# Performance work log

Measured on AMD Instinct MI355X. Metric: run time of the kernel, lower is better.

## Reference

```python
import jax, jax.numpy as jnp
import numpy as np
import math

E_IN, E_OUT = 512, 96
B, QL, PL = 64, 128, 196

def _lin(k, shape):
    fan_in = shape[1]
    bound = 1.0 / math.sqrt(fan_in)
    k1, k2 = jax.random.split(k)
    W = jax.random.uniform(k1, shape, jnp.float32, -bound, bound)
    b = jax.random.uniform(k2, (shape[0],), jnp.float32, -bound, bound)
    return W, b

def setup_inputs() -> dict:
    key = jax.random.key(0)
    ks = jax.random.split(key, 16)
    inp = {
        'z_d_cls': jax.random.normal(ks[0], (B, E_IN), jnp.float32),
        'Z_d_tok': jax.random.normal(ks[1], (B, QL, E_IN), jnp.float32),
        'z_t_cls': jax.random.normal(ks[2], (B, E_IN), jnp.float32),
        'Z_t_tok': jax.random.normal(ks[3], (B, QL, E_IN), jnp.float32),
        'z_v_cls': jax.random.normal(ks[4], (B, E_IN), jnp.float32),
        'Z_v_patch': jax.random.normal(ks[5], (B, PL, E_IN), jnp.float32),
    }
    names = ['t_cls', 'd_cls', 'v_cls', 't_tok', 'v_patch', 'tgl_q', 'tgl_k', 'tgl_v']
    for i, n in enumerate(names):
        W, b = _lin(ks[6 + i], (E_OUT, E_IN))
        inp[f'W_{n}'] = W
        inp[f'b_{n}'] = b
    inp['ln_g'] = jnp.ones((E_OUT,), jnp.float32)
    inp['ln_b'] = jnp.zeros((E_OUT,), jnp.float32)
    return inp

def _l2n(x, eps=1e-6):
    return x / jnp.maximum(jnp.linalg.norm(x, axis=-1, keepdims=True), eps)

def _proj(x, W, b):
    return x @ W.T + b

def _layer_norm(x, g, b, eps=1e-5):
    mu = jnp.mean(x, axis=-1, keepdims=True)
    var = jnp.mean((x - mu) ** 2, axis=-1, keepdims=True)
    return (x - mu) / jnp.sqrt(var + eps) * g + b

def reference(z_d_cls, Z_d_tok, z_t_cls, Z_t_tok, z_v_cls, Z_v_patch,
              W_t_cls, b_t_cls, W_d_cls, b_d_cls, W_v_cls, b_v_cls,
              W_t_tok, b_t_tok, W_v_patch, b_v_patch,
              W_tgl_q, b_tgl_q, W_tgl_k, b_tgl_k, W_tgl_v, b_tgl_v,
              ln_g, ln_b):
    # --- TGG: global-global text/doc cosine sim [B, B]
    t = _l2n(_proj(z_t_cls, W_t_cls, b_t_cls))
    d = _l2n(_proj(z_d_cls, W_d_cls, b_d_cls))
    S_TGG = t @ d.T
    # --- TGL: cross-attention over all batch pairs
    Q = _proj(Z_d_tok, W_tgl_q, b_tgl_q)   # [b, q, h]
    K = _proj(Z_t_tok, W_tgl_k, b_tgl_k)   # [c, k, h]
    V = _proj(Z_t_tok, W_tgl_v, b_tgl_v)   # [c, k, h]
    scores = jnp.einsum('bqh,ckh->bcqk', Q, K) / math.sqrt(E_OUT)
    attn = jax.nn.softmax(scores, axis=-1)
    context = jnp.einsum('bcqk,ckh->bcqh', attn, V).mean(axis=2)  # [b, c, h]
    context = _layer_norm(context, ln_g, ln_b)
    S_TGL = jnp.einsum('ih,ijh->ij', d, _l2n(context))
    S_TIB = 0.5 * (S_TGG + S_TGL)
    # --- CGG: global-global text/vision cosine sim
    v = _l2n(_proj(z_v_cls, W_v_cls, b_v_cls))
    S_CGG = t @ v.T
    # --- CLL: token-patch max similarity
    t_tok = _l2n(_proj(Z_t_tok, W_t_tok, b_t_tok))        # [b, t, h]
    v_pat = _l2n(_proj(Z_v_patch, W_v_patch, b_v_patch))  # [c, p, h]
    sim = jnp.einsum('bth,cph->bctp', t_tok, v_pat)
    S_CLL = sim.max(axis=(-1, -2))
    S_CAB = 0.5 * (S_CGG + S_CLL)
    return S_TIB + S_CAB
```

## Files before the change

### kernel.cpp

```cpp
#include <hip/hip_runtime.h>
#include <hip/hip_bf16.h>

typedef __bf16 bf16;
typedef __attribute__((ext_vector_type(8))) __bf16 bf16x8;
typedef __attribute__((ext_vector_type(4))) float f32x4;
typedef __attribute__((ext_vector_type(4))) unsigned int uint4v;

#define MFMA16(a, b, c) __builtin_amdgcn_mfma_f32_16x16x32_bf16(a, b, c, 0, 0, 0)

__device__ inline bf16x8 cvt8(const float* p) {
    f32x4 lo = *(const f32x4*)p;
    f32x4 hi = *(const f32x4*)(p + 4);
    bf16x8 r;
    r[0] = (bf16)lo[0]; r[1] = (bf16)lo[1]; r[2] = (bf16)lo[2]; r[3] = (bf16)lo[3];
    r[4] = (bf16)hi[0]; r[5] = (bf16)hi[1]; r[6] = (bf16)hi[2]; r[7] = (bf16)hi[3];
    return r;
}


struct WPtrs { const float* W[8]; };

__global__ __launch_bounds__(256) void cvtw_kernel(WPtrs wp, bf16* __restrict__ Wb) {
    int j   = blockIdx.x / 48;
    int blk = blockIdx.x - j * 48;
    int idx = (blk * 256 + threadIdx.x) * 4;
    f32x4 v = *(const f32x4*)(wp.W[j] + idx);
    bf16* dst = Wb + j * 49152 + idx;
    dst[0] = (bf16)v[0]; dst[1] = (bf16)v[1]; dst[2] = (bf16)v[2]; dst[3] = (bf16)v[3];
}


struct ProjParams {
    const float* src[8];
    const float* B[8];
    void* dst[8];
    const bf16* Wb;
};

__global__ __launch_bounds__(256, 3) void proj_kernel(ProjParams p) {
    int wid  = (blockIdx.x << 2) + (threadIdx.x >> 6);
    if (wid >= 1422) return;
    int lane = threadIdx.x & 63;
    int m = lane & 15, quad = lane >> 4;

    int job = 0, base = 0;
    if (wid >= 2)    { job = 1; base = 2; }
    if (wid >= 4)    { job = 2; base = 4; }
    if (wid >= 6)    { job = 3; base = 6; }
    if (wid >= 262)  { job = 4; base = 262; }
    if (wid >= 518)  { job = 5; base = 518; }
    if (wid >= 774)  { job = 6; base = 774; }
    if (wid >= 1030) { job = 7; base = 1030; }
    int wtile = wid - base;
    int r0 = wtile << 5;

    const float* X  = p.src[job];
    const bf16*  wb = p.Wb + job * 49152 + (size_t)m * 512 + quad * 8;
    const float* x0 = X + (size_t)(r0 + m) * 512 + quad * 8;
    const float* x1 = x0 + 16 * 512;

    f32x4 acc[2][6] = {};
    #pragma unroll 4
    for (int kk = 0; kk < 512; kk += 32) {
        bf16x8 a0 = cvt8(x0 + kk);
        bf16x8 a1 = cvt8(x1 + kk);
        #pragma unroll
        for (int nt = 0; nt < 6; nt++) {
            bf16x8 b = *(const bf16x8*)(wb + nt * 8192 + kk);
            acc[0][nt] = MFMA16(a0, b, acc[0][nt]);
            acc[1][nt] = MFMA16(a1, b, acc[1][nt]);
        }
    }
    const float* Bv = p.B[job];
    bool norm = (job < 3) || (job >= 6);
    #pragma unroll
    for (int t2 = 0; t2 < 2; t2++) {
        int row0 = r0 + t2 * 16;
        f32x4* a = acc[t2];
        #pragma unroll
        for (int nt = 0; nt < 6; nt++) {
            float bb = Bv[nt * 16 + m];
            a[nt][0] += bb; a[nt][1] += bb; a[nt][2] += bb; a[nt][3] += bb;
        }
        if (norm) {
            #pragma unroll
            for (int r = 0; r < 4; r++) {
                float ss = 0.0f;
                #pragma unroll
                for (int nt = 0; nt < 6; nt++) ss += a[nt][r] * a[nt][r];
                ss += __shfl_xor(ss, 1); ss += __shfl_xor(ss, 2);
                ss += __shfl_xor(ss, 4); ss += __shfl_xor(ss, 8);
                float inv = 1.0f / fmaxf(sqrtf(ss), 1e-6f);
                #pragma unroll
                for (int nt = 0; nt < 6; nt++) a[nt][r] *= inv;
            }
        }
        if (job < 3) {
            float* dst = (float*)p.dst[job];
            #pragma unroll
            for (int r = 0; r < 4; r++)
                #pragma unroll
                for (int nt = 0; nt < 6; nt++)
                    dst[(size_t)(row0 + quad * 4 + r) * 96 + nt * 16 + m] = a[nt][r];
        } else {
            bf16* dst = (bf16*)p.dst[job];
            #pragma unroll
            for (int r = 0; r < 4; r++)
                #pragma unroll
                for (int nt = 0; nt < 6; nt++)
                    dst[(size_t)(row0 + quad * 4 + r) * 96 + nt * 16 + m] = (bf16)a[nt][r];
        }
    }
}


__global__ __launch_bounds__(256, 3) void attn_kernel(
    const bf16* __restrict__ Qg, const bf16* __restrict__ Kg, const bf16* __restrict__ Vg,
    const float* __restrict__ dvec, const float* __restrict__ ln_g, const float* __restrict__ ln_b,
    float* __restrict__ S_TGL)
{
    int b = blockIdx.x >> 6, c = blockIdx.x & 63;
    int tid = threadIdx.x, lane = tid & 63, w = tid >> 6;
    int m = lane & 15, quad = lane >> 4;
    const bf16* Q = Qg + (size_t)b * (128 * 96);
    const bf16* K = Kg + (size_t)c * (128 * 96);
    const bf16* V = Vg + (size_t)c * (128 * 96);

    __shared__ __align__(16) bf16 Klds[128 * 96];
    #pragma unroll
    for (int ch = 0; ch < 6; ch++) {
        int idx = (ch * 256 + tid) * 8;
        *(uint4v*)(Klds + idx) = *(const uint4v*)(K + idx);
    }
    __syncthreads();

    f32x4 acc[2][8] = {};
    #pragma unroll
    for (int kk = 0; kk < 96; kk += 32) {
        bf16x8 a0 = *(const bf16x8*)(Q + (size_t)(w * 32 + m) * 96 + kk + quad * 8);
        bf16x8 a1 = *(const bf16x8*)(Q + (size_t)(w * 32 + 16 + m) * 96 + kk + quad * 8);
        #pragma unroll
        for (int nt = 0; nt < 8; nt++) {
            bf16x8 bb = *(const bf16x8*)(Klds + (nt * 16 + m) * 96 + kk + quad * 8);
            acc[0][nt] = MFMA16(a0, bb, acc[0][nt]);
            acc[1][nt] = MFMA16(a1, bb, acc[1][nt]);
        }
    }
    const float sc = 0.10206207261596575f;
    float wpart[8];
    #pragma unroll
    for (int nt = 0; nt < 8; nt++) wpart[nt] = 0.0f;
    #pragma unroll
    for (int mt = 0; mt < 2; mt++) {
        #pragma unroll
        for (int r = 0; r < 4; r++) {
            float tv[8]; float mx = -3.4e38f;
            #pragma unroll
            for (int nt = 0; nt < 8; nt++) { tv[nt] = acc[mt][nt][r] * sc; mx = fmaxf(mx, tv[nt]); }
            mx = fmaxf(mx, __shfl_xor(mx, 1)); mx = fmaxf(mx, __shfl_xor(mx, 2));
            mx = fmaxf(mx, __shfl_xor(mx, 4)); mx = fmaxf(mx, __shfl_xor(mx, 8));
            float s = 0.0f;
            #pragma unroll
            for (int nt = 0; nt < 8; nt++) { tv[nt] = __expf(tv[nt] - mx); s += tv[nt]; }
            s += __shfl_xor(s, 1); s += __shfl_xor(s, 2);
            s += __shfl_xor(s, 4); s += __shfl_xor(s, 8);
            float inv = 1.0f / s;
            #pragma unroll
            for (int nt = 0; nt < 8; nt++) wpart[nt] += tv[nt] * inv;
        }
    }
    #pragma unroll
    for (int nt = 0; nt < 8; nt++) {
        wpart[nt] += __shfl_xor(wpart[nt], 16);
        wpart[nt] += __shfl_xor(wpart[nt], 32);
    }
    __shared__ float wsum4[4][128];
    __shared__ float wk[128];
    __shared__ float ctx[96];
    if (lane < 16) {
        #pragma unroll
        for (int nt = 0; nt < 8; nt++) wsum4[w][nt * 16 + lane] = wpart[nt];
    }
    __syncthreads();
    if (tid < 128) wk[tid] = wsum4[0][tid] + wsum4[1][tid] + wsum4[2][tid] + wsum4[3][tid];
    __syncthreads();
    if (tid < 96) {
        float a = 0.0f;
        for (int k = 0; k < 128; k++) a += wk[k] * (float)V[(size_t)k * 96 + tid];
        ctx[tid] = a * (1.0f / 128.0f);
    }
    __syncthreads();
    if (w == 0) {
        float x0 = ctx[lane];
        float x1 = (lane < 32) ? ctx[64 + lane] : 0.0f;
        float s = x0 + x1;
        #pragma unroll
        for (int d = 1; d < 64; d <<= 1) s += __shfl_xor(s, d);
        float mean = s * (1.0f / 96.0f);
        float e0 = x0 - mean;
        float e1 = (lane < 32) ? (x1 - mean) : 0.0f;
        float q = e0 * e0 + e1 * e1;
        #pragma unroll
        for (int d = 1; d < 64; d <<= 1) q += __shfl_xor(q, d);
        float rstd = rsqrtf(q * (1.0f / 96.0f) + 1e-5f);
        float y0 = e0 * rstd * ln_g[lane] + ln_b[lane];
        float y1 = 0.0f;
        if (lane < 32) y1 = e1 * rstd * ln_g[64 + lane] + ln_b[64 + lane];
        const float* db = dvec + b * 96;
        float dot = y0 * db[lane] + ((lane < 32) ? y1 * db[64 + lane] : 0.0f);
        float ss = y0 * y0 + y1 * y1;
        #pragma unroll
        for (int d = 1; d < 64; d <<= 1) { dot += __shfl_xor(dot, d); ss += __shfl_xor(ss, d); }
        if (lane == 0) S_TGL[blockIdx.x] = dot / fmaxf(sqrtf(ss), 1e-6f);
    }
}


__global__ __launch_bounds__(256, 3) void cll_kernel(
    const bf16* __restrict__ Tt, const bf16* __restrict__ Vp, float* __restrict__ S_CLL)
{
    int b = blockIdx.x >> 6, c = blockIdx.x & 63;
    int tid = threadIdx.x, lane = tid & 63, w = tid >> 6;
    int m = lane & 15, quad = lane >> 4;
    const bf16* T = Tt + (size_t)b * (128 * 96);
    const bf16* P = Vp + (size_t)c * (196 * 96);

    __shared__ __align__(16) bf16 Plds[196 * 96];
    for (int ch = tid; ch < 2352; ch += 256)
        *(uint4v*)(Plds + ch * 8) = *(const uint4v*)(P + ch * 8);
    __syncthreads();

    int rofs[13];
    #pragma unroll
    for (int nt = 0; nt < 13; nt++) {
        int r = nt * 16 + m; if (r > 195) r = 195;
        rofs[nt] = r * 96;
    }
    f32x4 acc[2][13] = {};
    #pragma unroll
    for (int kk = 0; kk < 96; kk += 32) {
        bf16x8 a0 = *(const bf16x8*)(T + (size_t)(w * 32 + m) * 96 + kk + quad * 8);
        bf16x8 a1 = *(const bf16x8*)(T + (size_t)(w * 32 + 16 + m) * 96 + kk + quad * 8);
        #pragma unroll
        for (int nt = 0; nt < 13; nt++) {
            bf16x8 bb = *(const bf16x8*)(Plds + rofs[nt] + kk + quad * 8);
            acc[0][nt] = MFMA16(a0, bb, acc[0][nt]);
            acc[1][nt] = MFMA16(a1, bb, acc[1][nt]);
        }
    }
    float mx = -3.4e38f;
    #pragma unroll
    for (int mt = 0; mt < 2; mt++)
        #pragma unroll
        for (int nt = 0; nt < 13; nt++)
            #pragma unroll
            for (int r = 0; r < 4; r++) mx = fmaxf(mx, acc[mt][nt][r]);
    #pragma unroll
    for (int d = 1; d < 64; d <<= 1) mx = fmaxf(mx, __shfl_xor(mx, d));
    __shared__ float red[4];
    if (lane == 0) red[w] = mx;
    __syncthreads();
    if (tid == 0) S_CLL[blockIdx.x] = fmaxf(fmaxf(red[0], red[1]), fmaxf(red[2], red[3]));
}


__global__ __launch_bounds__(64) void final_kernel(
    const float* __restrict__ t, const float* __restrict__ d, const float* __restrict__ v,
    const float* __restrict__ S_TGL, const float* __restrict__ S_CLL, float* __restrict__ out)
{
    int i = blockIdx.x, j = threadIdx.x;
    __shared__ float ti[96];
    if (j < 64) ti[j] = t[i * 96 + j];
    if (j < 32) ti[64 + j] = t[i * 96 + 64 + j];
    __syncthreads();
    float tg = 0.0f, cg = 0.0f;
    const float* dj = d + j * 96;
    const float* vj = v + j * 96;
    #pragma unroll 8
    for (int h = 0; h < 96; h++) { float th = ti[h]; tg += th * dj[h]; cg += th * vj[h]; }
    float res = 0.5f * (tg + S_TGL[i * 64 + j]) + 0.5f * (cg + S_CLL[i * 64 + j]);
    out[i * 64 + j] = res;
}


extern "C" void kernel_launch(void* const* d_in, const int* in_sizes, int n_in,
                              void* d_out, int out_size, void* d_ws, size_t ws_size,
                              hipStream_t stream)
{
    (void)in_sizes; (void)n_in; (void)out_size; (void)ws_size;
    const float* z_d_cls   = (const float*)d_in[0];
    const float* Z_d_tok   = (const float*)d_in[1];
    const float* z_t_cls   = (const float*)d_in[2];
    const float* Z_t_tok   = (const float*)d_in[3];
    const float* z_v_cls   = (const float*)d_in[4];
    const float* Z_v_patch = (const float*)d_in[5];

    char* ws = (char*)d_ws;
    float* t     = (float*)(ws + 0);
    float* d     = (float*)(ws + 24576);
    float* v     = (float*)(ws + 49152);
    float* S_TGL = (float*)(ws + 73728);
    float* S_CLL = (float*)(ws + 90112);
    bf16* Wb = (bf16*)(ws + 106496);
    bf16* Qb = (bf16*)(ws + 892928);
    bf16* Kb = (bf16*)(ws + 892928 + 1572864);
    bf16* Vb = (bf16*)(ws + 892928 + 2 * 1572864);
    bf16* Tt = (bf16*)(ws + 892928 + 3 * 1572864);
    bf16* Vp = (bf16*)(ws + 892928 + 4 * 1572864);

    WPtrs wp;
    wp.W[0] = (const float*)d_in[6];
    wp.W[1] = (const float*)d_in[8];
    wp.W[2] = (const float*)d_in[10];
    wp.W[3] = (const float*)d_in[16];
    wp.W[4] = (const float*)d_in[18];
    wp.W[5] = (const float*)d_in[20];
    wp.W[6] = (const float*)d_in[12];
    wp.W[7] = (const float*)d_in[14];
    hipLaunchKernelGGL(cvtw_kernel, dim3(384), dim3(256), 0, stream, wp, Wb);

    ProjParams pp;
    pp.Wb = Wb;
    pp.src[0] = z_t_cls;   pp.B[0] = (const float*)d_in[7];  pp.dst[0] = t;
    pp.src[1] = z_d_cls;   pp.B[1] = (const float*)d_in[9];  pp.dst[1] = d;
    pp.src[2] = z_v_cls;   pp.B[2] = (const float*)d_in[11]; pp.dst[2] = v;
    pp.src[3] = Z_d_tok;   pp.B[3] = (const float*)d_in[17]; pp.dst[3] = Qb;
    pp.src[4] = Z_t_tok;   pp.B[4] = (const float*)d_in[19]; pp.dst[4] = Kb;
    pp.src[5] = Z_t_tok;   pp.B[5] = (const float*)d_in[21]; pp.dst[5] = Vb;
    pp.src[6] = Z_t_tok;   pp.B[6] = (const float*)d_in[13]; pp.dst[6] = Tt;
    pp.src[7] = Z_v_patch; pp.B[7] = (const float*)d_in[15]; pp.dst[7] = Vp;
    hipLaunchKernelGGL(proj_kernel, dim3(356), dim3(256), 0, stream, pp);

    hipLaunchKernelGGL(attn_kernel, dim3(4096), dim3(256), 0, stream,
                       (const bf16*)Qb, (const bf16*)Kb, (const bf16*)Vb,
                       (const float*)d, (const float*)d_in[22], (const float*)d_in[23], S_TGL);
    hipLaunchKernelGGL(cll_kernel, dim3(4096), dim3(256), 0, stream,
                       (const bf16*)Tt, (const bf16*)Vp, S_CLL);
    hipLaunchKernelGGL(final_kernel, dim3(64), dim3(64), 0, stream,
                       (const float*)t, (const float*)d, (const float*)v,
                       (const float*)S_TGL, (const float*)S_CLL, (float*)d_out);
}
```

Measured before the change: 254.1 us.

## Split projection N across two waves, pad LDS rows, parallelize attention V reduction

The projection kernel now uses 128-thread blocks in which two waves each compute half of the 96 output columns for a 32-row tile. The row L2 norm is combined across the two waves through shared memory, and the grid grows to 1422 blocks for more parallelism. The attention and CLL kernels pad their LDS rows from 96 to 104 bf16 elements to avoid bank conflicts on MFMA operand loads, and both drop the min-blocks occupancy hint. The attention context reduction over V now runs on all four waves with paired bf16 loads instead of a serial 128-step loop on 96 threads, at the cost of an extra sync and a small partial-sum buffer.

```diff
diff --git a/kernel.cpp b/kernel.cpp
--- a/kernel.cpp
+++ b/kernel.cpp
@@ -37,84 +37,105 @@
     const bf16* Wb;
 };
 
-__global__ __launch_bounds__(256, 3) void proj_kernel(ProjParams p) {
-    int wid  = (blockIdx.x << 2) + (threadIdx.x >> 6);
-    if (wid >= 1422) return;
-    int lane = threadIdx.x & 63;
+__global__ __launch_bounds__(128, 8) void proj_kernel(ProjParams p) {
+    int g   = blockIdx.x;
+    int tid = threadIdx.x;
+    int nh = tid >> 6, lane = tid & 63;
     int m = lane & 15, quad = lane >> 4;
 
     int job = 0, base = 0;
-    if (wid >= 2)    { job = 1; base = 2; }
-    if (wid >= 4)    { job = 2; base = 4; }
-    if (wid >= 6)    { job = 3; base = 6; }
-    if (wid >= 262)  { job = 4; base = 262; }
-    if (wid >= 518)  { job = 5; base = 518; }
-    if (wid >= 774)  { job = 6; base = 774; }
-    if (wid >= 1030) { job = 7; base = 1030; }
-    int wtile = wid - base;
-    int r0 = wtile << 5;
+    if (g >= 2)    { job = 1; base = 2; }
+    if (g >= 4)    { job = 2; base = 4; }
+    if (g >= 6)    { job = 3; base = 6; }
+    if (g >= 262)  { job = 4; base = 262; }
+    if (g >= 518)  { job = 5; base = 518; }
+    if (g >= 774)  { job = 6; base = 774; }
+    if (g >= 1030) { job = 7; base = 1030; }
+    int r0 = (g - base) << 5;
 
     const float* X  = p.src[job];
-    const bf16*  wb = p.Wb + job * 49152 + (size_t)m * 512 + quad * 8;
+    const bf16*  wb = p.Wb + job * 49152 + (size_t)(nh * 48 + m) * 512 + quad * 8;
     const float* x0 = X + (size_t)(r0 + m) * 512 + quad * 8;
     const float* x1 = x0 + 16 * 512;
 
-    f32x4 acc[2][6] = {};
+    f32x4 acc[2][3] = {};
     #pragma unroll 4
     for (int kk = 0; kk < 512; kk += 32) {
         bf16x8 a0 = cvt8(x0 + kk);
         bf16x8 a1 = cvt8(x1 + kk);
         #pragma unroll
-        for (int nt = 0; nt < 6; nt++) {
+        for (int nt = 0; nt < 3; nt++) {
             bf16x8 b = *(const bf16x8*)(wb + nt * 8192 + kk);
             acc[0][nt] = MFMA16(a0, b, acc[0][nt]);
             acc[1][nt] = MFMA16(a1, b, acc[1][nt]);
         }
     }
     const float* Bv = p.B[job];
+    #pragma unroll
+    for (int t2 = 0; t2 < 2; t2++)
+        #pragma unroll
+        for (int nt = 0; nt < 3; nt++) {
+            float bb = Bv[nh * 48 + nt * 16 + m];
+            acc[t2][nt][0] += bb; acc[t2][nt][1] += bb;
+            acc[t2][nt][2] += bb; acc[t2][nt][3] += bb;
+        }
+
     bool norm = (job < 3) || (job >= 6);
-    #pragma unroll
-    for (int t2 = 0; t2 < 2; t2++) {
-        int row0 = r0 + t2 * 16;
-        f32x4* a = acc[t2];
-        #pragma unroll
-        for (int nt = 0; nt < 6; nt++) {
-            float bb = Bv[nt * 16 + m];
-            a[nt][0] += bb; a[nt][1] += bb; a[nt][2] += bb; a[nt][3] += bb;
-        }
-        if (norm) {
+    __shared__ float sx[2][2][16];
+    if (norm) {
+        float ss[2][4];
+        #pragma unroll
+        for (int t2 = 0; t2 < 2; t2++)
             #pragma unroll
             for (int r = 0; r < 4; r++) {
-                float ss = 0.0f;
-                #pragma unroll
-                for (int nt = 0; nt < 6; nt++) ss += a[nt][r] * a[nt][r];
-                ss += __shfl_xor(ss, 1); ss += __shfl_xor(ss, 2);
-                ss += __shfl_xor(ss, 4); ss += __shfl_xor(ss, 8);
-                float inv = 1.0f / fmaxf(sqrtf(ss), 1e-6f);
-                #pragma unroll
-                for (int nt = 0; nt < 6; nt++) a[nt][r] *= inv;
+                float s = 0.0f;
+                #pragma unroll
+                for (int nt = 0; nt < 3; nt++) s += acc[t2][nt][r] * acc[t2][nt][r];
+                s += __shfl_xor(s, 1); s += __shfl_xor(s, 2);
+                s += __shfl_xor(s, 4); s += __shfl_xor(s, 8);
+                ss[t2][r] = s;
             }
-        }
-        if (job < 3) {
-            float* dst = (float*)p.dst[job];
+        if (m == 0) {
+            #pragma unroll
+            for (int t2 = 0; t2 < 2; t2++)
+                #pragma unroll
+                for (int r = 0; r < 4; r++)
+                    sx[nh][t2][quad * 4 + r] = ss[t2][r];
+        }
+        __syncthreads();
+        #pragma unroll
+        for (int t2 = 0; t2 < 2; t2++)
+            #pragma unroll
+            for (int r = 0; r < 4; r++) {
+                float tot = ss[t2][r] + sx[1 - nh][t2][quad * 4 + r];
+                float inv = 1.0f / fmaxf(sqrtf(tot), 1e-6f);
+                #pragma unroll
+                for (int nt = 0; nt < 3; nt++) acc[t2][nt][r] *= inv;
+            }
+    }
+    if (job < 3) {
+        float* dst = (float*)p.dst[job];
+        #pragma unroll
+        for (int t2 = 0; t2 < 2; t2++)
             #pragma unroll
             for (int r = 0; r < 4; r++)
                 #pragma unroll
-                for (int nt = 0; nt < 6; nt++)
-                    dst[(size_t)(row0 + quad * 4 + r) * 96 + nt * 16 + m] = a[nt][r];
-        } else {
-            bf16* dst = (bf16*)p.dst[job];
+                for (int nt = 0; nt < 3; nt++)
+                    dst[(size_t)(r0 + t2 * 16 + quad * 4 + r) * 96 + nh * 48 + nt * 16 + m] = acc[t2][nt][r];
+    } else {
+        bf16* dst = (bf16*)p.dst[job];
+        #pragma unroll
+        for (int t2 = 0; t2 < 2; t2++)
             #pragma unroll
             for (int r = 0; r < 4; r++)
                 #pragma unroll
-                for (int nt = 0; nt < 6; nt++)
-                    dst[(size_t)(row0 + quad * 4 + r) * 96 + nt * 16 + m] = (bf16)a[nt][r];
-        }
-    }
-}
-
-
-__global__ __launch_bounds__(256, 3) void attn_kernel(
+                for (int nt = 0; nt < 3; nt++)
+                    dst[(size_t)(r0 + t2 * 16 + quad * 4 + r) * 96 + nh * 48 + nt * 16 + m] = (bf16)acc[t2][nt][r];
+    }
+}
+
+
+__global__ __launch_bounds__(256) void attn_kernel(
     const bf16* __restrict__ Qg, const bf16* __restrict__ Kg, const bf16* __restrict__ Vg,
     const float* __restrict__ dvec, const float* __restrict__ ln_g, const float* __restrict__ ln_b,
     float* __restrict__ S_TGL)
@@ -126,11 +147,12 @@
     const bf16* K = Kg + (size_t)c * (128 * 96);
     const bf16* V = Vg + (size_t)c * (128 * 96);
 
-    __shared__ __align__(16) bf16 Klds[128 * 96];
-    #pragma unroll
-    for (int ch = 0; ch < 6; ch++) {
-        int idx = (ch * 256 + tid) * 8;
-        *(uint4v*)(Klds + idx) = *(const uint4v*)(K + idx);
+    __shared__ __align__(16) bf16 Klds[128 * 104];
+    #pragma unroll
+    for (int it = 0; it < 6; it++) {
+        int ch = it * 256 + tid;
+        int row = ch / 12, seg = ch - row * 12;
+        *(uint4v*)(Klds + row * 104 + seg * 8) = *(const uint4v*)(K + ch * 8);
     }
     __syncthreads();
 
@@ -141,7 +163,7 @@
         bf16x8 a1 = *(const bf16x8*)(Q + (size_t)(w * 32 + 16 + m) * 96 + kk + quad * 8);
         #pragma unroll
         for (int nt = 0; nt < 8; nt++) {
-            bf16x8 bb = *(const bf16x8*)(Klds + (nt * 16 + m) * 96 + kk + quad * 8);
+            bf16x8 bb = *(const bf16x8*)(Klds + (nt * 16 + m) * 104 + kk + quad * 8);
             acc[0][nt] = MFMA16(a0, bb, acc[0][nt]);
             acc[1][nt] = MFMA16(a1, bb, acc[1][nt]);
         }
@@ -176,6 +198,7 @@
     }
     __shared__ float wsum4[4][128];
     __shared__ float wk[128];
+    __shared__ float ctxp[4][96];
     __shared__ float ctx[96];
     if (lane < 16) {
         #pragma unroll
@@ -184,11 +207,24 @@
     __syncthreads();
     if (tid < 128) wk[tid] = wsum4[0][tid] + wsum4[1][tid] + wsum4[2][tid] + wsum4[3][tid];
     __syncthreads();
-    if (tid < 96) {
-        float a = 0.0f;
-        for (int k = 0; k < 128; k++) a += wk[k] * (float)V[(size_t)k * 96 + tid];
-        ctx[tid] = a * (1.0f / 128.0f);
-    }
+    {
+        float c0 = 0.0f, c1 = 0.0f;
+        if (lane < 48) {
+            #pragma unroll 4
+            for (int r = 0; r < 32; r++) {
+                int k = w * 32 + r;
+                unsigned u = *(const unsigned*)(V + (size_t)k * 96 + lane * 2);
+                float lo = __uint_as_float(u << 16);
+                float hi = __uint_as_float(u & 0xffff0000u);
+                float wkk = wk[k];
+                c0 += wkk * lo; c1 += wkk * hi;
+            }
+            ctxp[w][lane * 2]     = c0;
+            ctxp[w][lane * 2 + 1] = c1;
+        }
+    }
+    __syncthreads();
+    if (tid < 96) ctx[tid] = (ctxp[0][tid] + ctxp[1][tid] + ctxp[2][tid] + ctxp[3][tid]) * (1.0f / 128.0f);
     __syncthreads();
     if (w == 0) {
         float x0 = ctx[lane];
@@ -216,7 +252,7 @@
 }
 
 
-__global__ __launch_bounds__(256, 3) void cll_kernel(
+__global__ __launch_bounds__(256) void cll_kernel(
     const bf16* __restrict__ Tt, const bf16* __restrict__ Vp, float* __restrict__ S_CLL)
 {
     int b = blockIdx.x >> 6, c = blockIdx.x & 63;
@@ -225,16 +261,18 @@
     const bf16* T = Tt + (size_t)b * (128 * 96);
     const bf16* P = Vp + (size_t)c * (196 * 96);
 
-    __shared__ __align__(16) bf16 Plds[196 * 96];
-    for (int ch = tid; ch < 2352; ch += 256)
-        *(uint4v*)(Plds + ch * 8) = *(const uint4v*)(P + ch * 8);
+    __shared__ __align__(16) bf16 Plds[196 * 104];
+    for (int ch = tid; ch < 2352; ch += 256) {
+        int row = ch / 12, seg = ch - row * 12;
+        *(uint4v*)(Plds + row * 104 + seg * 8) = *(const uint4v*)(P + ch * 8);
+    }
     __syncthreads();
 
     int rofs[13];
     #pragma unroll
     for (int nt = 0; nt < 13; nt++) {
         int r = nt * 16 + m; if (r > 195) r = 195;
-        rofs[nt] = r * 96;
+        rofs[nt] = r * 104;
     }
     f32x4 acc[2][13] = {};
     #pragma unroll
@@ -329,7 +367,7 @@
     pp.src[5] = Z_t_tok;   pp.B[5] = (const float*)d_in[21]; pp.dst[5] = Vb;
     pp.src[6] = Z_t_tok;   pp.B[6] = (const float*)d_in[13]; pp.dst[6] = Tt;
     pp.src[7] = Z_v_patch; pp.B[7] = (const float*)d_in[15]; pp.dst[7] = Vp;
-    hipLaunchKernelGGL(proj_kernel, dim3(356), dim3(256), 0, stream, pp);
+    hipLaunchKernelGGL(proj_kernel, dim3(1422), dim3(128), 0, stream, pp);
 
     hipLaunchKernelGGL(attn_kernel, dim3(4096), dim3(256), 0, stream,
                        (const bf16*)Qb, (const bf16*)Kb, (const bf16*)Vb,
```

After: 243.9 us. 1.04x faster.
